# Kernel tuning notes

Measured on AMD Instinct MI355X. Metric: run time of the kernel, lower is better.

Reference implementation:

```python
import jax, jax.numpy as jnp
import numpy as np
from jax import lax

B, CIN, COUT, K, MOD, BANK = 4, 64, 32, 3, 128, 4
D = H = W = 32
EPS = 1e-8


def _lin_upsample2x(x, axis):
    n = x.shape[axis]
    dst = jnp.arange(2 * n, dtype=jnp.float32)
    src = jnp.maximum((dst + 0.5) * 0.5 - 0.5, 0.0)
    i0 = jnp.floor(src).astype(jnp.int32)
    i1 = jnp.minimum(i0 + 1, n - 1)
    w1 = src - i0.astype(jnp.float32)
    shape = [1] * x.ndim
    shape[axis] = 2 * n
    w1 = w1.reshape(shape)
    return jnp.take(x, i0, axis=axis) * (1.0 - w1) + jnp.take(x, i1, axis=axis) * w1


def upsample_trilinear2x(x):
    for ax in (2, 3, 4):
        x = _lin_upsample2x(x, ax)
    return x


def setup_inputs() -> dict:
    key = jax.random.key(0)
    ks = jax.random.split(key, 9)
    fan = CIN * K * K * K
    return {
        "x": jax.random.normal(ks[0], (B, CIN, D, H, W), jnp.float32),
        "style": jax.random.normal(ks[1], (B, MOD), jnp.float32),
        "bank": jax.random.normal(ks[2], (BANK, COUT, CIN, K, K, K), jnp.float32) / np.sqrt(fan),
        "affine_w": jax.random.normal(ks[3], (CIN, MOD), jnp.float32) / np.sqrt(MOD),
        "affine_b": jnp.ones((CIN,), jnp.float32),  # StyleGAN bias init = 1
        "sel_w": jax.random.normal(ks[4], (BANK, MOD), jnp.float32) / np.sqrt(MOD),
        "sel_b": jnp.zeros((BANK,), jnp.float32),
        "vox_w": jax.random.normal(ks[5], (1, COUT), jnp.float32) / np.sqrt(COUT),
        "vox_b": jnp.zeros((1,), jnp.float32),
    }


def reference(x, style, bank, affine_w, affine_b, sel_w, sel_b, vox_w, vox_b):
    # --- AdaptiveModulatedConv3d: select kernel from bank, modulate, demodulate ---
    alpha = jax.nn.softmax(style @ sel_w.T + sel_b, axis=-1)            # [B, BANK]
    w = jnp.einsum('bn,noidhw->boidhw', alpha, bank)                    # per-sample kernel
    s = style @ affine_w.T + affine_b                                   # [B, CIN]
    w = w * s[:, None, :, None, None, None]                             # modulate
    demod = lax.rsqrt(jnp.sum(w * w, axis=(2, 3, 4, 5)) + EPS)          # [B, COUT]
    w = w * demod[:, :, None, None, None, None]

    def conv1(xi, wi):
        return lax.conv_general_dilated(
            xi[None], wi, window_strides=(1, 1, 1),
            padding=[(1, 1), (1, 1), (1, 1)],
            dimension_numbers=('NCDHW', 'OIDHW', 'NCDHW'))[0]

    y = jax.vmap(conv1)(x, w)                                           # [B, COUT, D, H, W]

    y = upsample_trilinear2x(y)                                         # [B, COUT, 2D, 2H, 2W]

    # --- VoxelizingBlock: 1x1x1 conv to 1 channel ---
    out = jnp.einsum('oc,bcdhw->bodhw', vox_w, y) + vox_b[None, :, None, None, None]
    return (y, out)
```

## Files before the change

kernel.cpp:

```cpp
#include <hip/hip_runtime.h>
#include <math.h>

#define B_    4
#define CIN_  64
#define COUT_ 32
#define MOD_  128
#define VOX_  32768
#define UPVOX_ 262144
#define TAPS_ 27
#define EPS_  1e-8f

#define HALO_   1224
#define XUNITS_ 2448
#define WUNITS_ 1728
#define CHUNK_HALVES_ 13824

#define WS_ALPHA 0
#define WS_S     16
#define WS_WF16  512
#define WS_Y     111104
#define WS_V32   4305408

#define OUT_YUP  0
#define OUT_VOX  33554432

typedef _Float16 half8 __attribute__((ext_vector_type(8)));
typedef float floatx16 __attribute__((ext_vector_type(16)));

__global__ __launch_bounds__(256) void k_style(
    const float* __restrict__ style,
    const float* __restrict__ affine_w,
    const float* __restrict__ affine_b,
    const float* __restrict__ sel_w,
    const float* __restrict__ sel_b,
    float* __restrict__ ws) {
  __shared__ float lg[16];
  const int tid = threadIdx.x;

  if (tid < 16) {
    const int b = tid >> 2, n = tid & 3;
    float l = sel_b[n];
    for (int k = 0; k < MOD_; ++k) l += style[b * MOD_ + k] * sel_w[n * MOD_ + k];
    lg[tid] = l;
  }
  __syncthreads();
  if (tid < 16) {
    const int b = tid >> 2;
    const float m = fmaxf(fmaxf(lg[b * 4 + 0], lg[b * 4 + 1]),
                          fmaxf(lg[b * 4 + 2], lg[b * 4 + 3]));
    float den = 0.f;
    for (int j = 0; j < 4; ++j) den += expf(lg[b * 4 + j] - m);
    ws[WS_ALPHA + tid] = expf(lg[tid] - m) / den;
  }
  {
    const int b = tid >> 6, i = tid & 63;
    float v = affine_b[i];
    for (int k = 0; k < MOD_; ++k) v += style[b * MOD_ + k] * affine_w[i * MOD_ + k];
    ws[WS_S + tid] = v;
  }
}

__global__ __launch_bounds__(256) void k_weights(
    const float* __restrict__ bank,
    const float* __restrict__ ws_in,
    _Float16* __restrict__ wf) {
  const int b = blockIdx.x >> 5;
  const int o = blockIdx.x & 31;
  const int tid = threadIdx.x;
  __shared__ float red[256];

  float al[4];
#pragma unroll
  for (int n = 0; n < 4; ++n) al[n] = ws_in[WS_ALPHA + b * 4 + n];
  const float* sB = ws_in + WS_S + b * 64;

  float wv[7];
  float ss = 0.f;
#pragma unroll
  for (int r = 0; r < 7; ++r) {
    const int e = tid + r * 256;
    float v = 0.f;
    if (e < CIN_ * TAPS_) {
      const int i = e / TAPS_;
      const int t = e - i * TAPS_;
      const int base = (o * CIN_ + i) * TAPS_ + t;
      float bw = 0.f;
#pragma unroll
      for (int n = 0; n < 4; ++n)
        bw += al[n] * bank[base + n * (COUT_ * CIN_ * TAPS_)];
      v = bw * sB[i];
    }
    wv[r] = v;
    ss += v * v;
  }
  red[tid] = ss;
  __syncthreads();
  for (int st = 128; st > 0; st >>= 1) {
    if (tid < st) red[tid] += red[tid + st];
    __syncthreads();
  }
  const float demod = rsqrtf(red[0] + EPS_);

#pragma unroll
  for (int r = 0; r < 7; ++r) {
    const int e = tid + r * 256;
    if (e < CIN_ * TAPS_) {
      const int i = e / TAPS_;
      const int t = e - i * TAPS_;
      const int c = i >> 4, h = (i >> 3) & 1, j = i & 7;
      wf[((((b * 4 + c) * TAPS_ + t) * 2 + h) * 32 + o) * 8 + j] =
          (_Float16)(wv[r] * demod);
    }
  }
}

__global__ __launch_bounds__(256) void k_pack(
    const float* __restrict__ x, _Float16* __restrict__ xt) {
  const int yp = blockIdx.x, zp = blockIdx.y, b = blockIdx.z;
  const int gz = zp - 1, gy = yp - 1;
  const bool zy_ok = ((unsigned)gz < 32u) && ((unsigned)gy < 32u);
  const int gzc = min(max(gz, 0), 31);
  const int gyc = min(max(gy, 0), 31);
  _Float16* dst = xt + (((size_t)(b * 34 + zp) * 34 + yp) * 34) * 64;
  const float* srow = x + ((size_t)b * CIN_) * VOX_ + gzc * 1024 + gyc * 32;
  for (int u = threadIdx.x; u < 34 * 8; u += 256) {
    const int xp = u >> 3, q = u & 7;
    const int gx = xp - 1;
    const bool ok = zy_ok && ((unsigned)gx < 32u);
    const float m = ok ? 1.0f : 0.0f;
    const int gxc = min(max(gx, 0), 31);
    half8 h;
#pragma unroll
    for (int i = 0; i < 8; ++i) {
      const float v = srow[(size_t)(q * 8 + i) * VOX_ + gxc];
      h[i] = (_Float16)(v * m);
    }
    *(half8*)&dst[xp * 64 + q * 8] = h;
  }
}

__global__ __launch_bounds__(256, 1) void k_conv(
    const _Float16* __restrict__ xt,
    const _Float16* __restrict__ wf,
    const float* __restrict__ vox_w,
    float* __restrict__ ws_y,
    float* __restrict__ v32) {
  __shared__ __align__(16) _Float16 wl[2][CHUNK_HALVES_];
  __shared__ __align__(16) _Float16 xs[2][XUNITS_ * 8];

  const int b  = blockIdx.y;
  const int bx = blockIdx.x;
  const int z0 = (bx >> 3) * 4;
  const int y0 = (bx & 7) * 4;
  const int tid = threadIdx.x;
  const int w = tid >> 6;
  const int lane = tid & 63;
  const int hf = lane >> 5;
  const int col = lane & 31;
  const int wz = (w >> 1) * 2;
  const int wy = (w & 1) * 2;

  const _Float16* xtb = xt + (size_t)b * (34 * 34 * 34 * 64);
  const _Float16* wfb = wf + (size_t)b * 4 * CHUNK_HALVES_;

  int xoff[10];
  bool xok[10];
#pragma unroll
  for (int j = 0; j < 10; ++j) {
    const int u = j * 256 + tid;
    xok[j] = (u < XUNITS_);
    const int uc = xok[j] ? u : 0;
    const int h = uc / HALO_, hv = uc - h * HALO_;
    const int hz = hv / 204;
    const int rem = hv - hz * 204;
    const int hy = rem / 34;
    const int hx = rem - hy * 34;
    xoff[j] = (((z0 + hz) * 34 + (y0 + hy)) * 34 + hx) * 64 + h * 8;
  }

  floatx16 acc[2][2];
#pragma unroll
  for (int az = 0; az < 2; ++az)
#pragma unroll
    for (int ay = 0; ay < 2; ++ay)
#pragma unroll
      for (int r = 0; r < 16; ++r) acc[az][ay][r] = 0.f;

  half8 wv[7], xv[10];

  auto load_chunk = [&](int c) {
    const _Float16* wsrc = wfb + (size_t)c * CHUNK_HALVES_;
#pragma unroll
    for (int j = 0; j < 7; ++j) {
      const int u = j * 256 + tid;
      wv[j] = *(const half8*)(wsrc + (size_t)(u < WUNITS_ ? u : 0) * 8);
    }
#pragma unroll
    for (int j = 0; j < 10; ++j)
      xv[j] = *(const half8*)(xtb + xoff[j] + c * 16);
  };
  auto write_chunk = [&](int bufi) {
#pragma unroll
    for (int j = 0; j < 7; ++j) {
      const int u = j * 256 + tid;
      if (u < WUNITS_) *(half8*)&wl[bufi][u * 8] = wv[j];
    }
#pragma unroll
    for (int j = 0; j < 10; ++j) {
      const int u = j * 256 + tid;
      if (xok[j]) *(half8*)&xs[bufi][u * 8] = xv[j];
    }
  };
  auto compute = [&](int bufi) {
    const _Float16* xb_ = xs[bufi];
    const _Float16* wb_ = wl[bufi];
#pragma unroll
    for (int dx = 0; dx < 3; ++dx) {
      half8 Bf[4][4];
#pragma unroll
      for (int zs = 0; zs < 4; ++zs)
#pragma unroll
        for (int ys = 0; ys < 4; ++ys) {
          const int hv = ((wz + zs) * 6 + (wy + ys)) * 34 + dx + col;
          Bf[zs][ys] = *(const half8*)&xb_[(hf * HALO_ + hv) * 8];
        }
#pragma unroll
      for (int dz = 0; dz < 3; ++dz)
#pragma unroll
        for (int dy = 0; dy < 3; ++dy) {
          const int t = (dz * 3 + dy) * 3 + dx;
          const half8 af = *(const half8*)&wb_[((t * 2 + hf) * 32 + col) * 8];
          acc[0][0] = __builtin_amdgcn_mfma_f32_32x32x16_f16(af, Bf[dz][dy], acc[0][0], 0, 0, 0);
          acc[0][1] = __builtin_amdgcn_mfma_f32_32x32x16_f16(af, Bf[dz][dy + 1], acc[0][1], 0, 0, 0);
          acc[1][0] = __builtin_amdgcn_mfma_f32_32x32x16_f16(af, Bf[dz + 1][dy], acc[1][0], 0, 0, 0);
          acc[1][1] = __builtin_amdgcn_mfma_f32_32x32x16_f16(af, Bf[dz + 1][dy + 1], acc[1][1], 0, 0, 0);
        }
    }
  };

  load_chunk(0);
  write_chunk(0);
  __syncthreads();
  for (int c = 0; c < 4; ++c) {
    if (c < 3) load_chunk(c + 1);
    compute(c & 1);
    if (c < 3) {
      write_chunk((c + 1) & 1);
      __syncthreads();
    }
  }

  float vw[16];
#pragma unroll
  for (int r = 0; r < 16; ++r)
    vw[r] = vox_w[(r & 3) + 8 * (r >> 2) + 4 * hf];

  float* yb2 = ws_y + (size_t)b * COUT_ * VOX_;
#pragma unroll
  for (int az = 0; az < 2; ++az)
#pragma unroll
    for (int ay = 0; ay < 2; ++ay) {
      const int zz = z0 + wz + az, yy = y0 + wy + ay;
      const int vbase = zz * 1024 + yy * 32 + col;
      float p = 0.f;
#pragma unroll
      for (int r = 0; r < 16; ++r) {
        const int oc = (r & 3) + 8 * (r >> 2) + 4 * hf;
        yb2[(size_t)oc * VOX_ + vbase] = acc[az][ay][r];
        p = fmaf(vw[r], acc[az][ay][r], p);
      }
      p += __shfl_xor(p, 32);
      if (hf == 0) v32[((size_t)b << 15) + vbase] = p;
    }
}

__global__ __launch_bounds__(256) void k_up(
    const float* __restrict__ ws_y,
    const float* __restrict__ v32,
    const float* __restrict__ vox_b,
    float* __restrict__ out) {
  __shared__ float P[3][1056];
  const int kz = blockIdx.x;
  const int ch = blockIdx.y;
  const int b = blockIdx.z;

  const int pzm = max(kz - 1, 0), pzp = min(kz + 1, 31);
  const float* src = (ch < 32) ? (ws_y + (((size_t)(b * 32 + ch)) << 15))
                               : (v32 + ((size_t)b << 15));
  for (int j = threadIdx.x; j < 768; j += 256) {
    const int p = j >> 8, idx = j & 255;
    const int r = idx >> 3, q = (idx & 7) * 4;
    const int zsrc = (p == 0) ? pzm : ((p == 1) ? kz : pzp);
    const float4 v = *(const float4*)(src + (zsrc << 10) + r * 32 + q);
    float* dp = &P[p][r * 33 + q];
    dp[0] = v.x; dp[1] = v.y; dp[2] = v.z; dp[3] = v.w;
  }
  __syncthreads();

  const int yp = threadIdx.x >> 3;
  const int xq = threadIdx.x & 7;
  const int ym = max(yp - 1, 0) * 33, yc = yp * 33, ypp = min(yp + 1, 31) * 33;

  int gxi[6];
#pragma unroll
  for (int i = 0; i < 6; ++i) gxi[i] = min(max(4 * xq - 1 + i, 0), 31);

  float ry[3][2][6];
#pragma unroll
  for (int p = 0; p < 3; ++p)
#pragma unroll
    for (int i = 0; i < 6; ++i) {
      const float a = P[p][ym + gxi[i]];
      const float bb = P[p][yc + gxi[i]];
      const float cc = P[p][ypp + gxi[i]];
      ry[p][0][i] = fmaf(0.25f, a, 0.75f * bb);
      ry[p][1][i] = fmaf(0.25f, cc, 0.75f * bb);
    }

  const float vb = (ch == 32) ? vox_b[0] : 0.f;
  float* base = out + ((ch < 32) ? (OUT_YUP + (((size_t)(b * 32 + ch)) * UPVOX_))
                                 : (OUT_VOX + (size_t)b * UPVOX_)) +
                (size_t)(2 * kz) * 4096 + (2 * yp) * 64 + 8 * xq;

#pragma unroll
  for (int zo = 0; zo < 2; ++zo)
#pragma unroll
    for (int yo = 0; yo < 2; ++yo) {
      float s[6];
#pragma unroll
      for (int i = 0; i < 6; ++i)
        s[i] = zo == 0 ? fmaf(0.25f, ry[0][yo][i], 0.75f * ry[1][yo][i])
                       : fmaf(0.25f, ry[2][yo][i], 0.75f * ry[1][yo][i]);
      float o[8];
#pragma unroll
      for (int ox = 0; ox < 8; ++ox) {
        const int k = ox >> 1;
        o[ox] = (ox & 1) ? fmaf(0.25f, s[k + 2], 0.75f * s[k + 1])
                         : fmaf(0.25f, s[k], 0.75f * s[k + 1]);
        o[ox] += vb;
      }
      float4* dst = (float4*)(base + (size_t)zo * 4096 + yo * 64);
      float4 v0; v0.x = o[0]; v0.y = o[1]; v0.z = o[2]; v0.w = o[3];
      float4 v1; v1.x = o[4]; v1.y = o[5]; v1.z = o[6]; v1.w = o[7];
      dst[0] = v0;
      dst[1] = v1;
    }
}

extern "C" void kernel_launch(void* const* d_in, const int* in_sizes, int n_in,
                              void* d_out, int out_size, void* d_ws, size_t ws_size,
                              hipStream_t stream) {
  const float* x        = (const float*)d_in[0];
  const float* style    = (const float*)d_in[1];
  const float* bank     = (const float*)d_in[2];
  const float* affine_w = (const float*)d_in[3];
  const float* affine_b = (const float*)d_in[4];
  const float* sel_w    = (const float*)d_in[5];
  const float* sel_b    = (const float*)d_in[6];
  const float* vox_w    = (const float*)d_in[7];
  const float* vox_b    = (const float*)d_in[8];
  float* out = (float*)d_out;
  float* ws  = (float*)d_ws;
  _Float16* wf16 = (_Float16*)(ws + WS_WF16);
  float* ws_y = ws + WS_Y;
  float* v32  = ws + WS_V32;
  _Float16* xt = (_Float16*)d_out;

  k_style<<<1, 256, 0, stream>>>(style, affine_w, affine_b, sel_w, sel_b, ws);
  k_weights<<<128, 256, 0, stream>>>(bank, ws, wf16);
  k_pack<<<dim3(34, 34, B_), 256, 0, stream>>>(x, xt);
  k_conv<<<dim3(64, B_), 256, 0, stream>>>(xt, wf16, vox_w, ws_y, v32);
  k_up<<<dim3(32, 33, B_), 256, 0, stream>>>(ws_y, v32, vox_b, out);
}
```

Measured before the change: 233.4 us.

## Halve conv tile depth, read weights from global, double blocks and occupancy

Each conv block now covers 2 z-slices instead of 4, so the grid doubles to 128x4 blocks and launch bounds allow 2 blocks per CU. Weight fragments are no longer staged through LDS; each MFMA operand is loaded straight from global memory or cache. This cuts the LDS footprint and register pressure and gives more parallelism across CUs. The cost is more halo re-reads per output and repeated global weight loads inside the inner loop, plus half the MFMA reuse of each weight fragment.

```diff
diff --git a/kernel.cpp b/kernel.cpp
--- a/kernel.cpp
+++ b/kernel.cpp
@@ -10,9 +10,8 @@
 #define TAPS_ 27
 #define EPS_  1e-8f
 
-#define HALO_   1224
-#define XUNITS_ 2448
-#define WUNITS_ 1728
+#define HALO_   816
+#define XUNITS_ 1632
 #define CHUNK_HALVES_ 13824
 
 #define WS_ALPHA 0
@@ -139,34 +138,33 @@
   }
 }
 
-__global__ __launch_bounds__(256, 1) void k_conv(
+__global__ __launch_bounds__(256, 2) void k_conv(
     const _Float16* __restrict__ xt,
     const _Float16* __restrict__ wf,
     const float* __restrict__ vox_w,
     float* __restrict__ ws_y,
     float* __restrict__ v32) {
-  __shared__ __align__(16) _Float16 wl[2][CHUNK_HALVES_];
   __shared__ __align__(16) _Float16 xs[2][XUNITS_ * 8];
 
   const int b  = blockIdx.y;
   const int bx = blockIdx.x;
-  const int z0 = (bx >> 3) * 4;
+  const int z0 = (bx >> 3) * 2;
   const int y0 = (bx & 7) * 4;
   const int tid = threadIdx.x;
   const int w = tid >> 6;
   const int lane = tid & 63;
   const int hf = lane >> 5;
   const int col = lane & 31;
-  const int wz = (w >> 1) * 2;
+  const int lz = w >> 1;
   const int wy = (w & 1) * 2;
 
   const _Float16* xtb = xt + (size_t)b * (34 * 34 * 34 * 64);
   const _Float16* wfb = wf + (size_t)b * 4 * CHUNK_HALVES_;
 
-  int xoff[10];
-  bool xok[10];
-#pragma unroll
-  for (int j = 0; j < 10; ++j) {
+  int xoff[7];
+  bool xok[7];
+#pragma unroll
+  for (int j = 0; j < 7; ++j) {
     const int u = j * 256 + tid;
     xok[j] = (u < XUNITS_);
     const int uc = xok[j] ? u : 0;
@@ -178,63 +176,47 @@
     xoff[j] = (((z0 + hz) * 34 + (y0 + hy)) * 34 + hx) * 64 + h * 8;
   }
 
-  floatx16 acc[2][2];
-#pragma unroll
-  for (int az = 0; az < 2; ++az)
-#pragma unroll
-    for (int ay = 0; ay < 2; ++ay)
-#pragma unroll
-      for (int r = 0; r < 16; ++r) acc[az][ay][r] = 0.f;
-
-  half8 wv[7], xv[10];
+  floatx16 acc[2];
+#pragma unroll
+  for (int ay = 0; ay < 2; ++ay)
+#pragma unroll
+    for (int r = 0; r < 16; ++r) acc[ay][r] = 0.f;
+
+  half8 xv[7];
 
   auto load_chunk = [&](int c) {
-    const _Float16* wsrc = wfb + (size_t)c * CHUNK_HALVES_;
-#pragma unroll
-    for (int j = 0; j < 7; ++j) {
-      const int u = j * 256 + tid;
-      wv[j] = *(const half8*)(wsrc + (size_t)(u < WUNITS_ ? u : 0) * 8);
-    }
-#pragma unroll
-    for (int j = 0; j < 10; ++j)
+#pragma unroll
+    for (int j = 0; j < 7; ++j)
       xv[j] = *(const half8*)(xtb + xoff[j] + c * 16);
   };
   auto write_chunk = [&](int bufi) {
 #pragma unroll
     for (int j = 0; j < 7; ++j) {
       const int u = j * 256 + tid;
-      if (u < WUNITS_) *(half8*)&wl[bufi][u * 8] = wv[j];
-    }
-#pragma unroll
-    for (int j = 0; j < 10; ++j) {
-      const int u = j * 256 + tid;
       if (xok[j]) *(half8*)&xs[bufi][u * 8] = xv[j];
     }
   };
-  auto compute = [&](int bufi) {
+  auto compute = [&](int bufi, int c) {
     const _Float16* xb_ = xs[bufi];
-    const _Float16* wb_ = wl[bufi];
+    const _Float16* wc = wfb + (size_t)c * CHUNK_HALVES_ + (hf * 32 + col) * 8;
 #pragma unroll
     for (int dx = 0; dx < 3; ++dx) {
-      half8 Bf[4][4];
-#pragma unroll
-      for (int zs = 0; zs < 4; ++zs)
-#pragma unroll
-        for (int ys = 0; ys < 4; ++ys) {
-          const int hv = ((wz + zs) * 6 + (wy + ys)) * 34 + dx + col;
-          Bf[zs][ys] = *(const half8*)&xb_[(hf * HALO_ + hv) * 8];
+#pragma unroll
+      for (int dz = 0; dz < 3; ++dz) {
+        half8 Bf[4];
+#pragma unroll
+        for (int r = 0; r < 4; ++r) {
+          const int hv = ((lz + dz) * 6 + (wy + r)) * 34 + dx + col;
+          Bf[r] = *(const half8*)&xb_[(hf * HALO_ + hv) * 8];
         }
-#pragma unroll
-      for (int dz = 0; dz < 3; ++dz)
 #pragma unroll
         for (int dy = 0; dy < 3; ++dy) {
           const int t = (dz * 3 + dy) * 3 + dx;
-          const half8 af = *(const half8*)&wb_[((t * 2 + hf) * 32 + col) * 8];
-          acc[0][0] = __builtin_amdgcn_mfma_f32_32x32x16_f16(af, Bf[dz][dy], acc[0][0], 0, 0, 0);
-          acc[0][1] = __builtin_amdgcn_mfma_f32_32x32x16_f16(af, Bf[dz][dy + 1], acc[0][1], 0, 0, 0);
-          acc[1][0] = __builtin_amdgcn_mfma_f32_32x32x16_f16(af, Bf[dz + 1][dy], acc[1][0], 0, 0, 0);
-          acc[1][1] = __builtin_amdgcn_mfma_f32_32x32x16_f16(af, Bf[dz + 1][dy + 1], acc[1][1], 0, 0, 0);
+          const half8 af = *(const half8*)(wc + t * 512);
+          acc[0] = __builtin_amdgcn_mfma_f32_32x32x16_f16(af, Bf[dy], acc[0], 0, 0, 0);
+          acc[1] = __builtin_amdgcn_mfma_f32_32x32x16_f16(af, Bf[dy + 1], acc[1], 0, 0, 0);
         }
+      }
     }
   };
 
@@ -243,7 +225,7 @@
   __syncthreads();
   for (int c = 0; c < 4; ++c) {
     if (c < 3) load_chunk(c + 1);
-    compute(c & 1);
+    compute(c & 1, c);
     if (c < 3) {
       write_chunk((c + 1) & 1);
       __syncthreads();
@@ -256,22 +238,21 @@
     vw[r] = vox_w[(r & 3) + 8 * (r >> 2) + 4 * hf];
 
   float* yb2 = ws_y + (size_t)b * COUT_ * VOX_;
-#pragma unroll
-  for (int az = 0; az < 2; ++az)
-#pragma unroll
-    for (int ay = 0; ay < 2; ++ay) {
-      const int zz = z0 + wz + az, yy = y0 + wy + ay;
-      const int vbase = zz * 1024 + yy * 32 + col;
-      float p = 0.f;
-#pragma unroll
-      for (int r = 0; r < 16; ++r) {
-        const int oc = (r & 3) + 8 * (r >> 2) + 4 * hf;
-        yb2[(size_t)oc * VOX_ + vbase] = acc[az][ay][r];
-        p = fmaf(vw[r], acc[az][ay][r], p);
-      }
-      p += __shfl_xor(p, 32);
-      if (hf == 0) v32[((size_t)b << 15) + vbase] = p;
-    }
+  const int zz = z0 + lz;
+#pragma unroll
+  for (int ay = 0; ay < 2; ++ay) {
+    const int yy = y0 + wy + ay;
+    const int vbase = zz * 1024 + yy * 32 + col;
+    float p = 0.f;
+#pragma unroll
+    for (int r = 0; r < 16; ++r) {
+      const int oc = (r & 3) + 8 * (r >> 2) + 4 * hf;
+      yb2[(size_t)oc * VOX_ + vbase] = acc[ay][r];
+      p = fmaf(vw[r], acc[ay][r], p);
+    }
+    p += __shfl_xor(p, 32);
+    if (hf == 0) v32[((size_t)b << 15) + vbase] = p;
+  }
 }
 
 __global__ __launch_bounds__(256) void k_up(
@@ -369,6 +350,6 @@
   k_style<<<1, 256, 0, stream>>>(style, affine_w, affine_b, sel_w, sel_b, ws);
   k_weights<<<128, 256, 0, stream>>>(bank, ws, wf16);
   k_pack<<<dim3(34, 34, B_), 256, 0, stream>>>(x, xt);
-  k_conv<<<dim3(64, B_), 256, 0, stream>>>(xt, wf16, vox_w, ws_y, v32);
+  k_conv<<<dim3(128, B_), 256, 0, stream>>>(xt, wf16, vox_w, ws_y, v32);
   k_up<<<dim3(32, 33, B_), 256, 0, stream>>>(ws_y, v32, vox_b, out);
 }
```

Measured after the change: 239.3 us. 1.03x slower.
